# Kernel optimization log

Hardware: AMD Instinct MI355X
Metric: run time of the kernel (lower is better)

The kernel has to match this reference:

```python
import jax, jax.numpy as jnp
import numpy as np

B, C, H, W = 64, 256, 14, 14
K = 9
HID = 256   # EdgeAgg hidden_channels = in_channels
OUT = 512   # out_channels = 2*in_channels (required by final reshape)


def _knn(q, kset, k):
    # ViG dense_knn_matrix: squared-distance knn, top-k of -dist (self-loop may be included)
    qs = jnp.sum(q * q, -1)
    ks = jnp.sum(kset * kset, -1)
    dist = qs[:, :, None] - 2.0 * jnp.einsum('bnc,bmc->bnm', q, kset) + ks[:, None, :]
    _, idx = jax.lax.top_k(-dist, k)   # (B,N,k) neighbor indices into kset
    return idx


def _edgeconv_add(feat, nbr, validf, w, b):
    # PyG EdgeConv(nn=Linear, aggr='add') with per-node valid-edge mask:
    #   out[i] = sum_{j in valid nbrs(i)} cat(x_i, x_j - x_i) @ w + b
    # nn is linear, so aggregate neighbor diffs BEFORE the matmul (same math, less traffic).
    Cf = feat.shape[-1]
    wa, wb = w[:Cf], w[Cf:]
    deg = jnp.sum(validf, -1, keepdims=True)                   # (B,N,1)
    xj = feat[jnp.arange(feat.shape[0])[:, None, None], nbr]   # (B,N,k,C) gather
    sum_xj = jnp.einsum('bnkc,bnk->bnc', xj, validf)
    return deg * (feat @ wa + b) + (sum_xj - deg * feat) @ wb


def _forward(x, fc1_w, fc1_b, fc2_w, fc2_b, fce_w, fce_b, inout_w, inout_b,
             attn_w, attn_b, upd_w, upd_b, kp_w, kp_b, enc_w, enc_b,
             mu_w, mu_b, dec_w, dec_b, T):
    k = dec_w.shape[-1]
    b_, c_, h_, w_ = x.shape
    n = h_ * w_
    xs = x.reshape(b_, c_, n)                       # (B,C,N)
    x_sp = jnp.transpose(xs, (0, 2, 1))             # (B,N,C) true spatial node feats for knn
    x_sp_d = jax.lax.stop_gradient(x_sp)            # original detaches before knn
    x_nbr = _knn(x_sp_d, x_sp_d, k)
    # temporal roll across the T frames of each clip
    y_sp = jnp.roll(x_sp.reshape(b_ // T, T, n, c_), -1, axis=1).reshape(b_, n, c_)
    y_nbr = _knn(x_sp_d, jax.lax.stop_gradient(y_sp), k)
    # faithful to original: x.view(B*N, C) reinterprets the contiguous (B,C,N) buffer
    x_feat = xs.reshape(b_, n, c_)
    y_feat = jnp.transpose(y_sp, (0, 2, 1)).reshape(b_, n, c_)
    # VAE-like K predictor (deterministic z = mu); argmax -> per-node degree in [0,k)
    hk = x_feat.reshape(b_ * n, c_) @ kp_w + kp_b
    hk = jax.nn.relu(hk @ enc_w + enc_b)
    mu = hk @ mu_w + mu_b
    logits = mu @ dec_w + dec_b                     # (B*N, k)
    k_int = jnp.argmax(logits, axis=1)
    # generate_mask: keep the first k_int[i] of node i's k edges
    validf = (jnp.arange(k)[None, :] < k_int[:, None]).astype(x.dtype).reshape(b_, n, k)

    def edge_agg(feat, nbr):
        h1 = jax.nn.relu(_edgeconv_add(feat, nbr, validf, fc1_w, fc1_b))
        h2 = _edgeconv_add(h1, nbr, validf, fc2_w, fc2_b)
        return (h2 @ fce_w + fce_b).reshape(b_ * n, -1)

    x_agg = edge_agg(x_feat, x_nbr)
    y_agg = edge_agg(y_feat, y_nbr)
    scores = (jnp.concatenate([x_agg, y_agg], -1) @ attn_w + attn_b)[:, 0]
    wgt = jax.nn.softmax(scores, axis=0)[:, None]   # softmax over ALL B*N nodes (as in source)
    fused = wgt * x_agg + (1.0 - wgt) * y_agg
    xin = x_feat.reshape(b_ * n, c_) @ inout_w + inout_b
    upd = jax.nn.relu(jnp.concatenate([xin, fused], -1) @ upd_w + upd_b)   # (B*N, 2C)
    return jnp.transpose(upd.reshape(b_, n, 2 * c_), (0, 2, 1)).reshape(b_, 2 * c_, h_, w_)


def setup_inputs():
    key = jax.random.key(0)
    ks = iter(jax.random.split(key, 32))

    def lin(i, o):
        return jax.random.normal(next(ks), (i, o), jnp.float32) / np.sqrt(i)

    def bias(o):
        return jax.random.normal(next(ks), (o,), jnp.float32) * 0.01

    return {
        'x': jax.random.normal(next(ks), (B, C, H, W), jnp.float32),
        'fc1_w': lin(2 * C, HID), 'fc1_b': bias(HID),
        'fc2_w': lin(2 * HID, HID), 'fc2_b': bias(HID),
        'fce_w': lin(HID, OUT), 'fce_b': bias(OUT),
        'inout_w': lin(C, OUT), 'inout_b': bias(OUT),
        'attn_w': lin(2 * OUT, 1), 'attn_b': bias(1),
        'upd_w': lin(2 * OUT, OUT), 'upd_b': bias(OUT),
        'kp_w': lin(C, 500), 'kp_b': bias(500),
        'enc_w': lin(500, 64), 'enc_b': bias(64),
        'mu_w': lin(64, 32), 'mu_b': bias(32),
        'dec_w': lin(32, K), 'dec_b': bias(K),
        'T': 16,
    }


def reference(x, fc1_w, fc1_b, fc2_w, fc2_b, fce_w, fce_b, inout_w, inout_b,
              attn_w, attn_b, upd_w, upd_b, kp_w, kp_b, enc_w, enc_b,
              mu_w, mu_b, dec_w, dec_b, T):
    return _forward(x, fc1_w, fc1_b, fc2_w, fc2_b, fce_w, fce_b, inout_w, inout_b,
                    attn_w, attn_b, upd_w, upd_b, kp_w, kp_b, enc_w, enc_b,
                    mu_w, mu_b, dec_w, dec_b, T)
```

## Files before the change

### kernel.cpp

```cpp
#include <hip/hip_runtime.h>
#include <cstddef>
#include <cstdint>

constexpr int BATCH = 64;
constexpr int CH    = 256;
constexpr int NPT   = 196;
constexpr int ROWS  = BATCH * NPT;
constexpr int BSTRIDE = CH * NPT;
constexpr int KNB   = 8;

typedef __bf16 bf16x8 __attribute__((ext_vector_type(8)));
typedef __bf16 bf16x4 __attribute__((ext_vector_type(4)));
typedef _Float16 f16x8 __attribute__((ext_vector_type(8)));
typedef float  f32x4  __attribute__((ext_vector_type(4)));
typedef unsigned long long u64;

__device__ __forceinline__ int src_batch(int b) {
    return (b & ~15) | ((b + 1) & 15);
}

__device__ __forceinline__ void gload_lds16(const void* g, void* l) {
    __builtin_amdgcn_global_load_lds(
        (const __attribute__((address_space(1))) void*)g,
        (__attribute__((address_space(3))) void*)l, 16, 0, 0);
}

__device__ __forceinline__ int xcd_swz(int lin, int nwg) {
    int q = nwg >> 3;
    return (lin & 7) * q + (lin >> 3);
}

__global__ __launch_bounds__(256) void front_kernel(const float* __restrict__ x,
        _Float16* __restrict__ XH, _Float16* __restrict__ XL,
        __bf16* __restrict__ XB, float* __restrict__ qs,
        const float* __restrict__ W1, const float* __restrict__ b1,
        const float* __restrict__ W2, const float* __restrict__ b2,
        int* __restrict__ kint, float* __restrict__ degf) {
    __shared__ __attribute__((aligned(16))) char smem[21056];
    int bid = blockIdx.x;
    int t = threadIdx.x;
    if (bid < 1024) {
        float (*tile)[65] = (float(*)[65])smem;
        int m0 = (bid & 3) * 64, c0 = ((bid >> 2) & 3) * 64, b = bid >> 4;
        const float* xb = x + (size_t)b * BSTRIDE;
        #pragma unroll
        for (int s = 0; s < 16; ++s) {
            int idx = s * 256 + t;
            int cc = idx >> 6, mm = idx & 63;
            int m = m0 + mm;
            float v = (m < NPT) ? xb[(size_t)(c0 + cc) * NPT + m] : 0.f;
            tile[cc][mm] = v;
            if (m < NPT)
                XB[(size_t)b * BSTRIDE + (size_t)(c0 + cc) * NPT + m] = (__bf16)v;
        }
        __syncthreads();
        #pragma unroll
        for (int s = 0; s < 16; ++s) {
            int idx = s * 256 + t;
            int mm = idx >> 6, cc = idx & 63;
            float v = tile[cc][mm];
            _Float16 h = (_Float16)v;
            size_t off = ((size_t)b * 256 + (m0 + mm)) * 256 + c0 + cc;
            XH[off] = h;
            XL[off] = (_Float16)(v - (float)h);
        }
    } else if (bid < 1088) {
        int b = bid - 1024;
        int m = t;
        if (m >= NPT) return;
        const float* xb = x + (size_t)b * BSTRIDE;
        float acc = 0.f;
        for (int c = 0; c < CH; ++c) {
            float v = xb[c * NPT + m];
            acc = fmaf(v, v, acc);
        }
        qs[b * NPT + m] = acc;
    } else {
        float (*xr)[256] = (float(*)[256])smem;
        float (*ebuf)[64] = (float(*)[64])(smem + 16384);
        float (*lg)[9]   = (float(*)[9])(smem + 20480);
        int r0 = (bid - 1088) * 16;
        const float4* xg = (const float4*)(x + (size_t)r0 * 256);
        float4* xs = (float4*)&xr[0][0];
        #pragma unroll
        for (int s = 0; s < 4; ++s) xs[s * 256 + t] = xg[s * 256 + t];
        __syncthreads();
        int w = t >> 6, l = t & 63;
        {
            float bb = b1[l];
            float a0 = bb, a1 = bb, a2 = bb, a3 = bb;
            const float* x0 = xr[w * 4 + 0];
            const float* x1 = xr[w * 4 + 1];
            const float* x2 = xr[w * 4 + 2];
            const float* x3 = xr[w * 4 + 3];
            for (int c = 0; c < 256; ++c) {
                float wv = W1[c * 64 + l];
                a0 = fmaf(x0[c], wv, a0);
                a1 = fmaf(x1[c], wv, a1);
                a2 = fmaf(x2[c], wv, a2);
                a3 = fmaf(x3[c], wv, a3);
            }
            ebuf[w * 4 + 0][l] = fmaxf(a0, 0.f);
            ebuf[w * 4 + 1][l] = fmaxf(a1, 0.f);
            ebuf[w * 4 + 2][l] = fmaxf(a2, 0.f);
            ebuf[w * 4 + 3][l] = fmaxf(a3, 0.f);
        }
        __syncthreads();
        int rr = t >> 4, cc = t & 15;
        if (cc < 9) {
            float acc = b2[cc];
            for (int j = 0; j < 64; ++j)
                acc = fmaf(ebuf[rr][j], W2[j * 9 + cc], acc);
            lg[rr][cc] = acc;
        }
        __syncthreads();
        if (cc == 0) {
            float best = lg[rr][0];
            int bi = 0;
            #pragma unroll
            for (int j = 1; j < 9; ++j)
                if (lg[rr][j] > best) { best = lg[rr][j]; bi = j; }
            kint[r0 + rr] = bi;
            degf[r0 + rr] = (float)bi;
        }
    }
}

__global__ __launch_bounds__(256) void gram_mfma(const _Float16* __restrict__ XH,
        const _Float16* __restrict__ XL, const float* __restrict__ qs,
        u64* __restrict__ cand) {
    __shared__ __attribute__((aligned(16))) char smem[128 * 132 * 4];
    _Float16* Ah = (_Float16*)smem;
    _Float16* Al = Ah + 128 * 64;
    _Float16* Bh = Al + 128 * 64;
    _Float16* Bl = Bh + 128 * 64;
    float* dst = (float*)smem;
    int lin = blockIdx.x + 2 * blockIdx.y + 4 * blockIdx.z;
    int nid = xcd_swz(lin, 512);
    int bx = nid & 1, by = (nid >> 1) & 1;
    int job = nid >> 2;
    int qb = (job < 64) ? job : job - 64;
    int kb = (job < 64) ? qb : src_batch(qb);
    int t = threadIdx.x, w = t >> 6, l = t & 63;
    int r0 = by * 128, c0 = bx * 128;
    int lr = l & 15, lg = l >> 4;
    int wr = (w >> 1) * 64, wc = (w & 1) * 64;
    const _Float16* qh = XH + (size_t)qb * 65536;
    const _Float16* ql = XL + (size_t)qb * 65536;
    const _Float16* kh = XH + (size_t)kb * 65536;
    const _Float16* kl = XL + (size_t)kb * 65536;
    f32x4 acc[4][4] = {};
    for (int k0 = 0; k0 < 256; k0 += 64) {
        #pragma unroll
        for (int i = 0; i < 4; ++i) {
            int row = (w * 4 + i) * 8 + (l >> 3);
            int c8 = l & 7;
            size_t goA = (size_t)(r0 + row) * 256 + k0 + c8 * 8;
            size_t goB = (size_t)(c0 + row) * 256 + k0 + c8 * 8;
            gload_lds16(qh + goA, Ah + (w * 4 + i) * 512);
            gload_lds16(ql + goA, Al + (w * 4 + i) * 512);
            gload_lds16(kh + goB, Bh + (w * 4 + i) * 512);
            gload_lds16(kl + goB, Bl + (w * 4 + i) * 512);
        }
        asm volatile("s_waitcnt vmcnt(0)" ::: "memory");
        __syncthreads();
        #pragma unroll
        for (int ks = 0; ks < 2; ++ks) {
            f16x8 ah[4], al[4], bh[4], bl[4];
            #pragma unroll
            for (int mi = 0; mi < 4; ++mi) {
                ah[mi] = *(const f16x8*)(Ah + (wr + mi * 16 + lr) * 64 + ks * 32 + lg * 8);
                al[mi] = *(const f16x8*)(Al + (wr + mi * 16 + lr) * 64 + ks * 32 + lg * 8);
            }
            #pragma unroll
            for (int ni = 0; ni < 4; ++ni) {
                bh[ni] = *(const f16x8*)(Bh + (wc + ni * 16 + lr) * 64 + ks * 32 + lg * 8);
                bl[ni] = *(const f16x8*)(Bl + (wc + ni * 16 + lr) * 64 + ks * 32 + lg * 8);
            }
            #pragma unroll
            for (int mi = 0; mi < 4; ++mi)
                #pragma unroll
                for (int ni = 0; ni < 4; ++ni) {
                    acc[mi][ni] = __builtin_amdgcn_mfma_f32_16x16x32_f16(
                        ah[mi], bh[ni], acc[mi][ni], 0, 0, 0);
                    acc[mi][ni] = __builtin_amdgcn_mfma_f32_16x16x32_f16(
                        ah[mi], bl[ni], acc[mi][ni], 0, 0, 0);
                    acc[mi][ni] = __builtin_amdgcn_mfma_f32_16x16x32_f16(
                        al[mi], bh[ni], acc[mi][ni], 0, 0, 0);
                }
        }
        __syncthreads();
    }
    const float* qsq = qs + qb * NPT;
    const float* qsk = qs + kb * NPT;
    float ksv[4];
    #pragma unroll
    for (int ni = 0; ni < 4; ++ni) {
        int col = c0 + wc + ni * 16 + lr;
        ksv[ni] = (col < NPT) ? qsk[col] : 0.f;
    }
    #pragma unroll
    for (int mi = 0; mi < 4; ++mi) {
        #pragma unroll
        for (int r = 0; r < 4; ++r) {
            int lrow = wr + mi * 16 + lg * 4 + r;
            int grow = r0 + lrow;
            float qq = (grow < NPT) ? qsq[grow] : 0.f;
            #pragma unroll
            for (int ni = 0; ni < 4; ++ni) {
                float dist = qq - 2.f * acc[mi][ni][r] + ksv[ni];
                dst[lrow * 132 + wc + ni * 16 + lr] = dist;
            }
        }
    }
    __syncthreads();
    {
        int lrow = t >> 1, half = t & 1;
        int grow = r0 + lrow;
        if (grow < NPT) {
            int tile = (c0 >> 6) + half;
            u64 kreg[8];
            #pragma unroll
            for (int p = 0; p < 8; ++p) kreg[p] = ~0ull;
            const float* rp = dst + lrow * 132 + half * 64;
            for (int s4 = 0; s4 < 16; ++s4) {
                f32x4 dv = *(const f32x4*)(rp + s4 * 4);
                #pragma unroll
                for (int e = 0; e < 4; ++e) {
                    int col = (tile << 6) + s4 * 4 + e;
                    unsigned u = __float_as_uint(dv[e]);
                    u = (u & 0x80000000u) ? ~u : (u | 0x80000000u);
                    u64 key = (col < NPT) ? (((u64)u << 32) | (unsigned)col) : ~0ull;
                    if (key < kreg[7]) {
                        #pragma unroll
                        for (int p = 0; p < 8; ++p) {
                            u64 mn = (key < kreg[p]) ? key : kreg[p];
                            u64 mx = (key < kreg[p]) ? kreg[p] : key;
                            kreg[p] = mn; key = mx;
                        }
                    }
                }
            }
            u64* cp = cand + (((size_t)job * NPT + grow) * 4 + tile) * 8;
            #pragma unroll
            for (int p = 0; p < 8; ++p) cp[p] = kreg[p];
        }
    }
}

__global__ __launch_bounds__(256) void topk_merge(const u64* __restrict__ cand,
                                                  int* __restrict__ nbr) {
    int rowid = blockIdx.x * 256 + threadIdx.x;
    const u64* c = cand + (size_t)rowid * 32;
    int p0 = 0, p1 = 0, p2 = 0, p3 = 0;
    #pragma unroll
    for (int it = 0; it < 8; ++it) {
        u64 v0 = c[p0], v1 = c[8 + p1], v2 = c[16 + p2], v3 = c[24 + p3];
        u64 best = v0; int bj = 0;
        if (v1 < best) { best = v1; bj = 1; }
        if (v2 < best) { best = v2; bj = 2; }
        if (v3 < best) { best = v3; bj = 3; }
        if (bj == 0) p0 = (p0 < 7) ? p0 + 1 : 7;
        else if (bj == 1) p1 = (p1 < 7) ? p1 + 1 : 7;
        else if (bj == 2) p2 = (p2 < 7) ? p2 + 1 : 7;
        else p3 = (p3 < 7) ? p3 + 1 : 7;
        nbr[(size_t)rowid * KNB + it] = (int)(best & 0xffffffffu);
    }
}

__global__ __launch_bounds__(256) void prep_weights(
        const float* __restrict__ fc1_w, const float* __restrict__ fc2_w,
        const float* __restrict__ fce_w, const float* __restrict__ upd_w,
        const float* __restrict__ kp_w, const float* __restrict__ kp_b,
        const float* __restrict__ enc_w, const float* __restrict__ enc_b,
        const float* __restrict__ mu_w, const float* __restrict__ mu_b,
        const float* __restrict__ dec_w, const float* __restrict__ dec_b,
        const float* __restrict__ inout_w, const float* __restrict__ inout_b,
        const float* __restrict__ upd_b,
        __bf16* __restrict__ W1catT, __bf16* __restrict__ W2catT,
        __bf16* __restrict__ fcet, __bf16* __restrict__ updC,
        float* __restrict__ KW1, float* __restrict__ kb1,
        float* __restrict__ KW2, float* __restrict__ kb2,
        float* __restrict__ bcomp) {
    __shared__ float tile[64][65];
    int bid = blockIdx.x;
    int t = threadIdx.x;
    if (bid < 64) {
        const float* W = (bid < 32) ? fc1_w : fc2_w;
        __bf16* WT = (bid < 32) ? W1catT : W2catT;
        int local = bid & 31;
        int n0 = (local >> 2) * 64, k0 = (local & 3) * 64;
        #pragma unroll
        for (int s = 0; s < 16; ++s) {
            int idx = s * 256 + t;
            int kk = idx >> 6, nn = idx & 63;
            float v;
            if (n0 < 256)
                v = W[(size_t)(k0 + kk) * 256 + n0 + nn] -
                    W[(size_t)(k0 + kk + 256) * 256 + n0 + nn];
            else
                v = W[(size_t)(k0 + kk + 256) * 256 + (n0 - 256) + nn];
            tile[kk][nn] = v;
        }
        __syncthreads();
        #pragma unroll
        for (int s = 0; s < 16; ++s) {
            int idx = s * 256 + t;
            int nn = idx >> 6, kk = idx & 63;
            WT[(size_t)(n0 + nn) * 256 + k0 + kk] = (__bf16)tile[kk][nn];
        }
    } else if (bid < 96) {
        int local = bid - 64;
        int n0 = (local >> 2) * 64, k0 = (local & 3) * 64;
        #pragma unroll
        for (int s = 0; s < 16; ++s) {
            int idx = s * 256 + t;
            int kk = idx >> 6, nn = idx & 63;
            tile[kk][nn] = fce_w[(size_t)(k0 + kk) * 512 + n0 + nn];
        }
        __syncthreads();
        #pragma unroll
        for (int s = 0; s < 16; ++s) {
            int idx = s * 256 + t;
            int nn = idx >> 6, kk = idx & 63;
            fcet[(size_t)(n0 + nn) * 256 + k0 + kk] = (__bf16)tile[kk][nn];
        }
    } else if (bid < 160) {
        int local = bid - 96;
        int k0 = (local >> 3) * 64, n0 = (local & 7) * 64;
        #pragma unroll
        for (int s = 0; s < 16; ++s) {
            int idx = s * 256 + t;
            int kk = idx >> 6, nn = idx & 63;
            tile[kk][nn] = upd_w[(size_t)(512 + k0 + kk) * 512 + n0 + nn];
        }
        __syncthreads();
        #pragma unroll
        for (int s = 0; s < 16; ++s) {
            int idx = s * 256 + t;
            int nn = idx >> 6, kk = idx & 63;
            updC[(size_t)(n0 + nn) * 768 + 256 + k0 + kk] = (__bf16)tile[kk][nn];
        }
    } else if (bid < 224) {
        int i = (bid - 160) * 4 + (t >> 6);
        int j = t & 63;
        double acc = 0.0;
        for (int k = 0; k < 500; ++k)
            acc += (double)kp_w[(size_t)i * 500 + k] * (double)enc_w[(size_t)k * 64 + j];
        KW1[i * 64 + j] = (float)acc;
    } else if (bid == 224) {
        int j = t;
        if (j < 64) {
            double acc = (double)enc_b[j];
            for (int k = 0; k < 500; ++k)
                acc += (double)kp_b[k] * (double)enc_w[(size_t)k * 64 + j];
            kb1[j] = (float)acc;
        }
    } else if (bid < 228) {
        int e = (bid - 225) * 256 + t;
        if (e < 576) {
            int i = e / 9, j = e - (e / 9) * 9;
            double acc = 0.0;
            for (int k = 0; k < 32; ++k)
                acc += (double)mu_w[(size_t)i * 32 + k] * (double)dec_w[(size_t)k * 9 + j];
            KW2[e] = (float)acc;
        } else if (e < 585) {
            int j = e - 576;
            double acc = (double)dec_b[j];
            for (int k = 0; k < 32; ++k)
                acc += (double)mu_b[k] * (double)dec_w[(size_t)k * 9 + j];
            kb2[j] = (float)acc;
        }
    } else if (bid < 740) {
        int e = (bid - 228) * 256 + t;
        int k = e >> 9, n = e & 511;
        double acc = 0.0;
        for (int j = 0; j < 512; ++j)
            acc += (double)inout_w[(size_t)k * 512 + j] * (double)upd_w[(size_t)j * 512 + n];
        updC[(size_t)n * 768 + k] = (__bf16)(float)acc;
    } else {
        int n = (bid - 740) * 256 + t;
        double acc = (double)upd_b[n];
        for (int j = 0; j < 512; ++j)
            acc += (double)inout_b[j] * (double)upd_w[(size_t)j * 512 + n];
        bcomp[n] = (float)acc;
    }
}

template<int STAGE, int RELU>
__global__ __launch_bounds__(256) void combine_kernel(const __bf16* __restrict__ P,
        const int* __restrict__ nbr, const int* __restrict__ kint_,
        const float* __restrict__ degf, const float* __restrict__ bias,
        __bf16* __restrict__ H) {
    int g = threadIdx.x >> 6, lane = threadIdx.x & 63;
    int nid = xcd_swz(blockIdx.x, 2 * ROWS / 4);
    int r = nid * 4 + g;
    int branch = (r >= ROWS);
    int rr = r - branch * ROWS;
    int b = rr / NPT, i = rr - b * NPT;
    size_t srow, mbase;
    if constexpr (STAGE == 1) {
        int fb = branch ? src_batch(b) : b;
        srow = (size_t)fb * NPT + i;
        mbase = (size_t)fb * NPT;
    } else {
        srow = (size_t)r;
        mbase = (size_t)branch * ROWS + (size_t)b * NPT;
    }
    const int* nb = nbr + (size_t)branch * ((size_t)ROWS * KNB) + (size_t)rr * KNB;
    bf16x4 sv = *(const bf16x4*)(P + srow * 512 + lane * 4);
    float4 bv = *(const float4*)(bias + lane * 4);
    float s0 = 0.f, s1 = 0.f, s2 = 0.f, s3 = 0.f;
    int kk = kint_[rr];
    for (int tt = 0; tt < kk; ++tt) {
        int m = nb[tt];
        bf16x4 v = *(const bf16x4*)(P + (mbase + m) * 512 + 256 + lane * 4);
        s0 += (float)v[0]; s1 += (float)v[1]; s2 += (float)v[2]; s3 += (float)v[3];
    }
    float dg = degf[rr];
    float o0 = fmaf(dg, (float)sv[0] + bv.x, s0);
    float o1 = fmaf(dg, (float)sv[1] + bv.y, s1);
    float o2 = fmaf(dg, (float)sv[2] + bv.z, s2);
    float o3 = fmaf(dg, (float)sv[3] + bv.w, s3);
    if constexpr (RELU) {
        o0 = fmaxf(o0, 0.f); o1 = fmaxf(o1, 0.f);
        o2 = fmaxf(o2, 0.f); o3 = fmaxf(o3, 0.f);
    }
    bf16x4 ov;
    ov[0] = (__bf16)o0; ov[1] = (__bf16)o1; ov[2] = (__bf16)o2; ov[3] = (__bf16)o3;
    *(bf16x4*)(H + (size_t)r * 256 + lane * 4) = ov;
}

template<int FLAGS, int CONCAT>
__global__ __launch_bounds__(256) void mfma_gemm(
    const __bf16* __restrict__ A0, const __bf16* __restrict__ A1,
    const __bf16* __restrict__ WT, const float* __restrict__ bias,
    float* __restrict__ Cf, __bf16* __restrict__ Cb, int K, int N,
    const float* __restrict__ aw, float* __restrict__ scp,
    const float* __restrict__ wgt) {
    constexpr int SMEMB = (FLAGS & 8) ? (128 * 129 * 4) : (2 * 128 * 64 * 2);
    __shared__ __attribute__((aligned(16))) char smem[SMEMB];
    __bf16* As = (__bf16*)smem;
    __bf16* Bs = As + 128 * 64;
    int lin = blockIdx.x + 4 * blockIdx.y;
    int nid = xcd_swz(lin, 4 * gridDim.y);
    int bx = nid & 3, by = nid >> 2;
    int t = threadIdx.x, w = t >> 6, l = t & 63;
    int r0 = by * 128, c0 = bx * 128;
    int lr = l & 15, lg = l >> 4;
    int wr = (w >> 1) * 64, wc = (w & 1) * 64;
    f32x4 acc[4][4] = {};
    for (int k0 = 0; k0 < K; k0 += 64) {
        #pragma unroll
        for (int i = 0; i < 4; ++i) {
            int row = (w * 4 + i) * 8 + (l >> 3);
            int c8 = l & 7;
            if constexpr (CONCAT == 2) {
                if (k0 < 256) {
                    gload_lds16(A0 + (size_t)(r0 + row) * 256 + k0 + c8 * 8,
                                As + (w * 4 + i) * 512);
                } else {
                    int kk2 = k0 - 256 + c8 * 8;
                    size_t gr = (size_t)(r0 + row);
                    bf16x8 xa = *(const bf16x8*)(A1 + gr * 512 + kk2);
                    bf16x8 ya = *(const bf16x8*)(A1 + ((size_t)ROWS + gr) * 512 + kk2);
                    float wv = wgt[gr];
                    bf16x8 mx;
                    #pragma unroll
                    for (int j = 0; j < 8; ++j)
                        mx[j] = (__bf16)(wv * (float)xa[j] + (1.f - wv) * (float)ya[j]);
                    *(bf16x8*)(As + (w * 4 + i) * 512 + l * 8) = mx;
                }
            } else {
                gload_lds16(A0 + (size_t)(r0 + row) * K + k0 + c8 * 8,
                            As + (w * 4 + i) * 512);
            }
            gload_lds16(WT + (size_t)(c0 + row) * K + k0 + c8 * 8,
                        Bs + (w * 4 + i) * 512);
        }
        asm volatile("s_waitcnt vmcnt(0)" ::: "memory");
        __syncthreads();
        #pragma unroll
        for (int ks = 0; ks < 2; ++ks) {
            bf16x8 af[4], bfr[4];
            #pragma unroll
            for (int mi = 0; mi < 4; ++mi)
                af[mi] = *(const bf16x8*)(As + (wr + mi * 16 + lr) * 64 + ks * 32 + lg * 8);
            #pragma unroll
            for (int ni = 0; ni < 4; ++ni)
                bfr[ni] = *(const bf16x8*)(Bs + (wc + ni * 16 + lr) * 64 + ks * 32 + lg * 8);
            #pragma unroll
            for (int mi = 0; mi < 4; ++mi)
                #pragma unroll
                for (int ni = 0; ni < 4; ++ni)
                    acc[mi][ni] = __builtin_amdgcn_mfma_f32_16x16x32_bf16(
                        af[mi], bfr[ni], acc[mi][ni], 0, 0, 0);
        }
        __syncthreads();
    }
    if constexpr ((FLAGS & 8) != 0) {
        float* tile = (float*)smem;
        #pragma unroll
        for (int mi = 0; mi < 4; ++mi)
            #pragma unroll
            for (int r = 0; r < 4; ++r) {
                int rrow = wr + mi * 16 + lg * 4 + r;
                #pragma unroll
                for (int ni = 0; ni < 4; ++ni) {
                    int ccol = wc + ni * 16 + lr;
                    float v = acc[mi][ni][r];
                    if (bias) v += bias[c0 + ccol];
                    if constexpr ((FLAGS & 1) != 0) v = fmaxf(v, 0.f);
                    tile[rrow * 129 + ccol] = v;
                }
            }
        __syncthreads();
        int cc = t >> 6, rr2 = t & 63;
        #pragma unroll
        for (int cs = 0; cs < 128; cs += 4) {
            #pragma unroll
            for (int h = 0; h < 2; ++h) {
                int row = r0 + rr2 + h * 64;
                int bb = row / NPT, ii = row - bb * NPT;
                Cf[((size_t)bb * 512 + (c0 + cc + cs)) * NPT + ii] =
                    tile[(rr2 + h * 64) * 129 + cc + cs];
            }
        }
    } else if constexpr ((FLAGS & 16) != 0) {
        int half = (r0 >= ROWS) ? 1 : 0;
        float ps[4][4] = {};
        #pragma unroll
        for (int mi = 0; mi < 4; ++mi)
            #pragma unroll
            for (int r = 0; r < 4; ++r) {
                int row = r0 + wr + mi * 16 + lg * 4 + r;
                #pragma unroll
                for (int ni = 0; ni < 4; ++ni) {
                    int col = c0 + wc + ni * 16 + lr;
                    float v = acc[mi][ni][r] + bias[col];
                    Cb[(size_t)row * N + col] = (__bf16)v;
                    ps[mi][r] = fmaf(v, aw[half * 512 + col], ps[mi][r]);
                }
            }
        #pragma unroll
        for (int m = 1; m <= 8; m <<= 1)
            #pragma unroll
            for (int mi = 0; mi < 4; ++mi)
                #pragma unroll
                for (int r = 0; r < 4; ++r)
                    ps[mi][r] += __shfl_xor(ps[mi][r], m, 64);
        if (lr == 0) {
            int slot = half * 8 + bx * 2 + (w & 1);
            #pragma unroll
            for (int mi = 0; mi < 4; ++mi)
                #pragma unroll
                for (int r = 0; r < 4; ++r) {
                    int sr = r0 - half * ROWS + wr + mi * 16 + lg * 4 + r;
                    scp[(size_t)slot * ROWS + sr] = ps[mi][r];
                }
        }
    } else {
        #pragma unroll
        for (int mi = 0; mi < 4; ++mi) {
            #pragma unroll
            for (int r = 0; r < 4; ++r) {
                int row = r0 + wr + mi * 16 + lg * 4 + r;
                #pragma unroll
                for (int ni = 0; ni < 4; ++ni) {
                    int col = c0 + wc + ni * 16 + lr;
                    float v = acc[mi][ni][r];
                    if (bias) v += bias[col];
                    if constexpr ((FLAGS & 1) != 0) v = fmaxf(v, 0.f);
                    if constexpr ((FLAGS & 4) != 0)
                        Cb[(size_t)row * N + col] = (__bf16)v;
                    else
                        Cf[(size_t)row * N + col] = v;
                }
            }
        }
    }
}

__global__ __launch_bounds__(256) void softmax_part(const float* __restrict__ scp,
        const float* __restrict__ ab, float* __restrict__ scores,
        float* __restrict__ mpart, float* __restrict__ spart) {
    __shared__ float red[256];
    int t = threadIdx.x;
    int sr = blockIdx.x * 256 + t;
    float s = ab[0];
    #pragma unroll
    for (int i = 0; i < 16; ++i) s += scp[(size_t)i * ROWS + sr];
    scores[sr] = s;
    red[t] = s; __syncthreads();
    for (int off = 128; off; off >>= 1) {
        if (t < off) red[t] = fmaxf(red[t], red[t + off]);
        __syncthreads();
    }
    float mb = red[0]; __syncthreads();
    red[t] = expf(s - mb); __syncthreads();
    for (int off = 128; off; off >>= 1) {
        if (t < off) red[t] += red[t + off];
        __syncthreads();
    }
    if (t == 0) { mpart[blockIdx.x] = mb; spart[blockIdx.x] = red[0]; }
}

__global__ __launch_bounds__(256) void softmax_fin(const float* __restrict__ mpart,
        const float* __restrict__ spart, const float* __restrict__ scores,
        float* __restrict__ wgt) {
    __shared__ float MS[2];
    if (threadIdx.x == 0) {
        float M = mpart[0];
        for (int i = 1; i < 49; ++i) M = fmaxf(M, mpart[i]);
        float S = 0.f;
        for (int i = 0; i < 49; ++i) S += spart[i] * expf(mpart[i] - M);
        MS[0] = M; MS[1] = S;
    }
    __syncthreads();
    float M = MS[0], denom = MS[1];
    for (int i = threadIdx.x; i < ROWS; i += 256)
        wgt[i] = expf(scores[i] - M) / denom;
}

extern "C" void kernel_launch(void* const* d_in, const int* in_sizes, int n_in,
                              void* d_out, int out_size, void* d_ws, size_t ws_size,
                              hipStream_t stream) {
    (void)in_sizes; (void)n_in; (void)out_size; (void)ws_size;
    const float* x       = (const float*)d_in[0];
    const float* fc1_w   = (const float*)d_in[1];
    const float* fc1_b   = (const float*)d_in[2];
    const float* fc2_w   = (const float*)d_in[3];
    const float* fc2_b   = (const float*)d_in[4];
    const float* fce_w   = (const float*)d_in[5];
    const float* fce_b   = (const float*)d_in[6];
    const float* inout_w = (const float*)d_in[7];
    const float* inout_b = (const float*)d_in[8];
    const float* attn_w  = (const float*)d_in[9];
    const float* attn_b  = (const float*)d_in[10];
    const float* upd_w   = (const float*)d_in[11];
    const float* upd_b   = (const float*)d_in[12];
    const float* kp_w    = (const float*)d_in[13];
    const float* kp_b    = (const float*)d_in[14];
    const float* enc_w   = (const float*)d_in[15];
    const float* enc_b   = (const float*)d_in[16];
    const float* mu_w    = (const float*)d_in[17];
    const float* mu_b    = (const float*)d_in[18];
    const float* dec_w   = (const float*)d_in[19];
    const float* dec_b   = (const float*)d_in[20];
    float* out = (float*)d_out;

    char* base = (char*)d_ws;
    size_t o = 0;
    auto alloc = [&](size_t bytes) -> void* {
        void* p = base + o;
        o += (bytes + 255) & ~(size_t)255;
        return p;
    };
    float* qs     = (float*)alloc(ROWS * 4);
    float* degf   = (float*)alloc(ROWS * 4);
    float* scores = (float*)alloc(ROWS * 4);
    float* wgt    = (float*)alloc(ROWS * 4);
    int*   kint   = (int*)  alloc(ROWS * 4);
    float* KW1    = (float*)alloc(256 * 64 * 4);
    float* kb1    = (float*)alloc(64 * 4);
    float* KW2    = (float*)alloc(64 * 9 * 4);
    float* kb2    = (float*)alloc(9 * 4);
    float* bcomp  = (float*)alloc(512 * 4);
    float* scp    = (float*)alloc((size_t)16 * ROWS * 4);
    float* mpart  = (float*)alloc(64 * 4);
    float* spart  = (float*)alloc(64 * 4);
    int*   nbr    = (int*)  alloc((size_t)128 * NPT * KNB * 4);
    u64*   cand   = (u64*)  alloc((size_t)128 * NPT * 4 * 8 * 8);
    char*  regD   = (char*) alloc((size_t)ROWS * 512 * 2);
    __bf16* XB    = (__bf16*)alloc((size_t)ROWS * 256 * 2);
    __bf16* H1    = (__bf16*)alloc((size_t)2 * ROWS * 256 * 2);
    __bf16* H2    = (__bf16*)alloc((size_t)2 * ROWS * 256 * 2);
    char*  regAGG = (char*) alloc((size_t)2 * ROWS * 512 * 4);
    __bf16* W1catT= (__bf16*)alloc((size_t)512 * 256 * 2);
    __bf16* W2catT= (__bf16*)alloc((size_t)512 * 256 * 2);
    __bf16* fcet  = (__bf16*)alloc((size_t)512 * 256 * 2);
    __bf16* updC  = (__bf16*)alloc((size_t)512 * 768 * 2);
    __bf16* P1buf = (__bf16*)regD;
    _Float16* XSPH = (_Float16*)regAGG;
    _Float16* XSPL = XSPH + (size_t)64 * 256 * 256;
    __bf16* P2buf = (__bf16*)regAGG;
    __bf16* AGGb  = (__bf16*)regAGG;
    __bf16* XAGGb = AGGb;

    prep_weights<<<742, 256, 0, stream>>>(fc1_w, fc2_w, fce_w, upd_w,
                                          kp_w, kp_b, enc_w, enc_b,
                                          mu_w, mu_b, dec_w, dec_b,
                                          inout_w, inout_b, upd_b,
                                          W1catT, W2catT, fcet, updC,
                                          KW1, kb1, KW2, kb2, bcomp);
    front_kernel<<<1872, 256, 0, stream>>>(x, XSPH, XSPL, XB, qs,
                                           KW1, kb1, KW2, kb2, kint, degf);

    gram_mfma<<<dim3(2, 2, 128), 256, 0, stream>>>(XSPH, XSPL, qs, cand);
    topk_merge<<<98, 256, 0, stream>>>(cand, nbr);

    mfma_gemm<4, 0><<<dim3(4, 98), 256, 0, stream>>>(
        XB, nullptr, W1catT, nullptr, nullptr, P1buf, 256, 512,
        nullptr, nullptr, nullptr);
    combine_kernel<1, 1><<<2 * ROWS / 4, 256, 0, stream>>>(
        P1buf, nbr, kint, degf, fc1_b, H1);

    mfma_gemm<4, 0><<<dim3(4, 196), 256, 0, stream>>>(
        H1, nullptr, W2catT, nullptr, nullptr, P2buf, 256, 512,
        nullptr, nullptr, nullptr);
    combine_kernel<2, 0><<<2 * ROWS / 4, 256, 0, stream>>>(
        P2buf, nbr, kint, degf, fc2_b, H2);

    mfma_gemm<20, 0><<<dim3(4, 196), 256, 0, stream>>>(
        H2, nullptr, fcet, fce_b, nullptr, AGGb, 256, 512,
        attn_w, scp, nullptr);

    softmax_part<<<49, 256, 0, stream>>>(scp, attn_b, scores, mpart, spart);
    softmax_fin<<<1, 256, 0, stream>>>(mpart, spart, scores, wgt);

    mfma_gemm<9, 2><<<dim3(4, 98), 256, 0, stream>>>(
        XB, XAGGb, updC, bcomp, out, nullptr, 768, 512,
        nullptr, nullptr, wgt);
}
```

Baseline: 241.5 us.

## Write full distance matrix to global and run top-k in separate kernel

The gram kernel now writes the full distance rows to a global scratch buffer (row stride 208) instead of staging them in LDS and running per-tile top-8 inside the same kernel. A new top-k kernel has four threads scan quarters of each row, then merges the four sorted lists in shared memory. This replaces the old cand/topk_merge pair, shrinks gram_mfma's LDS footprint and takes the serial selection tail out of the MFMA kernel. The cost is extra global traffic for the distance matrix (about 128*196*208 floats).

New measurement: 232.0 us. -3.9%, faster.

```diff
diff --git a/kernel.cpp b/kernel.cpp
--- a/kernel.cpp
+++ b/kernel.cpp
@@ -8,6 +8,7 @@
 constexpr int ROWS  = BATCH * NPT;
 constexpr int BSTRIDE = CH * NPT;
 constexpr int KNB   = 8;
+constexpr int DSTR  = 208;
 
 typedef __bf16 bf16x8 __attribute__((ext_vector_type(8)));
 typedef __bf16 bf16x4 __attribute__((ext_vector_type(4)));
@@ -128,13 +129,11 @@
 
 __global__ __launch_bounds__(256) void gram_mfma(const _Float16* __restrict__ XH,
         const _Float16* __restrict__ XL, const float* __restrict__ qs,
-        u64* __restrict__ cand) {
-    __shared__ __attribute__((aligned(16))) char smem[128 * 132 * 4];
-    _Float16* Ah = (_Float16*)smem;
-    _Float16* Al = Ah + 128 * 64;
-    _Float16* Bh = Al + 128 * 64;
-    _Float16* Bl = Bh + 128 * 64;
-    float* dst = (float*)smem;
+        float* __restrict__ Dw) {
+    __shared__ __attribute__((aligned(16))) _Float16 Ah[128 * 64];
+    __shared__ __attribute__((aligned(16))) _Float16 Al[128 * 64];
+    __shared__ __attribute__((aligned(16))) _Float16 Bh[128 * 64];
+    __shared__ __attribute__((aligned(16))) _Float16 Bl[128 * 64];
     int lin = blockIdx.x + 2 * blockIdx.y + 4 * blockIdx.z;
     int nid = xcd_swz(lin, 512);
     int bx = nid & 1, by = (nid >> 1) & 1;
@@ -203,68 +202,68 @@
     for (int mi = 0; mi < 4; ++mi) {
         #pragma unroll
         for (int r = 0; r < 4; ++r) {
-            int lrow = wr + mi * 16 + lg * 4 + r;
-            int grow = r0 + lrow;
-            float qq = (grow < NPT) ? qsq[grow] : 0.f;
+            if (r0 + wr + mi * 16 + r >= NPT) continue;
+            int grow = r0 + wr + mi * 16 + lg * 4 + r;
+            if (grow >= NPT) continue;
+            float qq = qsq[grow];
+            size_t rbase = ((size_t)job * NPT + grow) * DSTR;
             #pragma unroll
             for (int ni = 0; ni < 4; ++ni) {
-                float dist = qq - 2.f * acc[mi][ni][r] + ksv[ni];
-                dst[lrow * 132 + wc + ni * 16 + lr] = dist;
-            }
-        }
-    }
+                int col = c0 + wc + ni * 16 + lr;
+                if (col < NPT)
+                    Dw[rbase + col] = qq - 2.f * acc[mi][ni][r] + ksv[ni];
+            }
+        }
+    }
+}
+
+__global__ __launch_bounds__(256) void topk_kernel(const float* __restrict__ Dw,
+                                                   int* __restrict__ nbr) {
+    __shared__ u64 lists[64][4][8];
+    int t = threadIdx.x;
+    int lrow = t >> 2, q = t & 3;
+    int rowid = blockIdx.x * 64 + lrow;
+    const float* rp = Dw + (size_t)rowid * DSTR + q * 52;
+    u64 kreg[8];
+    #pragma unroll
+    for (int p = 0; p < 8; ++p) kreg[p] = ~0ull;
+    for (int s4 = 0; s4 < 13; ++s4) {
+        f32x4 dv = *(const f32x4*)(rp + s4 * 4);
+        #pragma unroll
+        for (int e = 0; e < 4; ++e) {
+            int col = q * 52 + s4 * 4 + e;
+            unsigned u = __float_as_uint(dv[e]);
+            u = (u & 0x80000000u) ? ~u : (u | 0x80000000u);
+            u64 key = (col < NPT) ? (((u64)u << 32) | (unsigned)col) : ~0ull;
+            if (key < kreg[7]) {
+                #pragma unroll
+                for (int p = 0; p < 8; ++p) {
+                    u64 mn = (key < kreg[p]) ? key : kreg[p];
+                    u64 mx = (key < kreg[p]) ? kreg[p] : key;
+                    kreg[p] = mn; key = mx;
+                }
+            }
+        }
+    }
+    #pragma unroll
+    for (int p = 0; p < 8; ++p) lists[lrow][q][p] = kreg[p];
     __syncthreads();
-    {
-        int lrow = t >> 1, half = t & 1;
-        int grow = r0 + lrow;
-        if (grow < NPT) {
-            int tile = (c0 >> 6) + half;
-            u64 kreg[8];
-            #pragma unroll
-            for (int p = 0; p < 8; ++p) kreg[p] = ~0ull;
-            const float* rp = dst + lrow * 132 + half * 64;
-            for (int s4 = 0; s4 < 16; ++s4) {
-                f32x4 dv = *(const f32x4*)(rp + s4 * 4);
-                #pragma unroll
-                for (int e = 0; e < 4; ++e) {
-                    int col = (tile << 6) + s4 * 4 + e;
-                    unsigned u = __float_as_uint(dv[e]);
-                    u = (u & 0x80000000u) ? ~u : (u | 0x80000000u);
-                    u64 key = (col < NPT) ? (((u64)u << 32) | (unsigned)col) : ~0ull;
-                    if (key < kreg[7]) {
-                        #pragma unroll
-                        for (int p = 0; p < 8; ++p) {
-                            u64 mn = (key < kreg[p]) ? key : kreg[p];
-                            u64 mx = (key < kreg[p]) ? kreg[p] : key;
-                            kreg[p] = mn; key = mx;
-                        }
-                    }
-                }
-            }
-            u64* cp = cand + (((size_t)job * NPT + grow) * 4 + tile) * 8;
-            #pragma unroll
-            for (int p = 0; p < 8; ++p) cp[p] = kreg[p];
-        }
-    }
-}
-
-__global__ __launch_bounds__(256) void topk_merge(const u64* __restrict__ cand,
-                                                  int* __restrict__ nbr) {
-    int rowid = blockIdx.x * 256 + threadIdx.x;
-    const u64* c = cand + (size_t)rowid * 32;
-    int p0 = 0, p1 = 0, p2 = 0, p3 = 0;
-    #pragma unroll
-    for (int it = 0; it < 8; ++it) {
-        u64 v0 = c[p0], v1 = c[8 + p1], v2 = c[16 + p2], v3 = c[24 + p3];
-        u64 best = v0; int bj = 0;
-        if (v1 < best) { best = v1; bj = 1; }
-        if (v2 < best) { best = v2; bj = 2; }
-        if (v3 < best) { best = v3; bj = 3; }
-        if (bj == 0) p0 = (p0 < 7) ? p0 + 1 : 7;
-        else if (bj == 1) p1 = (p1 < 7) ? p1 + 1 : 7;
-        else if (bj == 2) p2 = (p2 < 7) ? p2 + 1 : 7;
-        else p3 = (p3 < 7) ? p3 + 1 : 7;
-        nbr[(size_t)rowid * KNB + it] = (int)(best & 0xffffffffu);
+    if (q == 0) {
+        const u64* c = &lists[lrow][0][0];
+        int p0 = 0, p1 = 0, p2 = 0, p3 = 0;
+        #pragma unroll
+        for (int it = 0; it < 8; ++it) {
+            u64 v0 = c[p0], v1 = c[8 + p1], v2 = c[16 + p2], v3 = c[24 + p3];
+            u64 best = v0; int bj = 0;
+            if (v1 < best) { best = v1; bj = 1; }
+            if (v2 < best) { best = v2; bj = 2; }
+            if (v3 < best) { best = v3; bj = 3; }
+            if (bj == 0) p0 = (p0 < 7) ? p0 + 1 : 7;
+            else if (bj == 1) p1 = (p1 < 7) ? p1 + 1 : 7;
+            else if (bj == 2) p2 = (p2 < 7) ? p2 + 1 : 7;
+            else p3 = (p3 < 7) ? p3 + 1 : 7;
+            nbr[(size_t)rowid * KNB + it] = (int)(best & 0xffffffffu);
+        }
     }
 }
 
@@ -670,7 +669,6 @@
     float* mpart  = (float*)alloc(64 * 4);
     float* spart  = (float*)alloc(64 * 4);
     int*   nbr    = (int*)  alloc((size_t)128 * NPT * KNB * 4);
-    u64*   cand   = (u64*)  alloc((size_t)128 * NPT * 4 * 8 * 8);
     char*  regD   = (char*) alloc((size_t)ROWS * 512 * 2);
     __bf16* XB    = (__bf16*)alloc((size_t)ROWS * 256 * 2);
     __bf16* H1    = (__bf16*)alloc((size_t)2 * ROWS * 256 * 2);
@@ -683,6 +681,7 @@
     __bf16* P1buf = (__bf16*)regD;
     _Float16* XSPH = (_Float16*)regAGG;
     _Float16* XSPL = XSPH + (size_t)64 * 256 * 256;
+    float* Dw     = (float*)(regAGG + (size_t)17 * 1024 * 1024);
     __bf16* P2buf = (__bf16*)regAGG;
     __bf16* AGGb  = (__bf16*)regAGG;
     __bf16* XAGGb = AGGb;
@@ -696,8 +695,8 @@
     front_kernel<<<1872, 256, 0, stream>>>(x, XSPH, XSPL, XB, qs,
                                            KW1, kb1, KW2, kb2, kint, degf);
 
-    gram_mfma<<<dim3(2, 2, 128), 256, 0, stream>>>(XSPH, XSPL, qs, cand);
-    topk_merge<<<98, 256, 0, stream>>>(cand, nbr);
+    gram_mfma<<<dim3(2, 2, 128), 256, 0, stream>>>(XSPH, XSPL, qs, Dw);
+    topk_kernel<<<392, 256, 0, stream>>>(Dw, nbr);
 
     mfma_gemm<4, 0><<<dim3(4, 98), 256, 0, stream>>>(
         XB, nullptr, W1catT, nullptr, nullptr, P1buf, 256, 512,
```
